# Performance work log

Measured on AMD Instinct MI355X. Metric: run time of the kernel, lower is better.

The kernel has to match this reference:

```python
import jax, jax.numpy as jnp
import numpy as np

TASKS = 32768          # init kwarg `tasks`
N_HEADS = TASKS + 1    # tasks + 1 distilled/shared head
IN_DIM, HID, OUT = 3, 100, 5


def setup_inputs() -> dict:
    key = jax.random.key(0)
    kx, k1, kb1, k2, kb2 = jax.random.split(key, 5)
    # per-task stacked parameters (equivalent to ModuleList of Linears)
    x = jax.random.normal(kx, (N_HEADS, IN_DIM), dtype=jnp.float32)
    # init scale ~ PyTorch default: U(-1/sqrt(fan_in), 1/sqrt(fan_in)); gaussian approx fine
    W1 = jax.random.normal(k1, (N_HEADS, HID, IN_DIM), dtype=jnp.float32) * (1.0 / np.sqrt(IN_DIM))
    b1 = jax.random.normal(kb1, (N_HEADS, HID), dtype=jnp.float32) * (1.0 / np.sqrt(IN_DIM))
    W2 = jax.random.normal(k2, (N_HEADS, OUT, HID), dtype=jnp.float32) * (1.0 / np.sqrt(HID))
    b2 = jax.random.normal(kb2, (N_HEADS, OUT), dtype=jnp.float32) * (1.0 / np.sqrt(HID))
    return {"x": x, "W1": W1, "b1": b1, "W2": W2, "b2": b2}


def reference(x, W1, b1, W2, b2):
    # x: (T+1, 3) -- one state vector per task head (matches x.view(tasks+1, -1))
    T1 = W1.shape[0]
    x = x.reshape(T1, -1)                                   # (T+1, 3)
    h = jax.nn.relu(jnp.einsum('thi,ti->th', W1, x) + b1)   # (T+1, 100)
    logits = jnp.einsum('toh,th->to', W2, h) + b2           # (T+1, 5)
    return jax.nn.softmax(logits, axis=-1)                  # (T+1, 5)
```

## Files before the change

### kernel.cpp

```cpp
#include <hip/hip_runtime.h>
#include <math.h>


#define N_HEADS 32769
#define IN_DIM  3
#define HID     100
#define OUT     5

__global__ __launch_bounds__(256) void distral_kernel(
    const float* __restrict__ x,
    const float* __restrict__ W1,
    const float* __restrict__ b1,
    const float* __restrict__ W2,
    const float* __restrict__ b2,
    float* __restrict__ out)
{
    const int wave = threadIdx.x >> 6;
    const int lane = threadIdx.x & 63;
    const int head = blockIdx.x * 4 + wave;
    if (head >= N_HEADS) return;

    const float x0 = x[head * 3 + 0];
    const float x1 = x[head * 3 + 1];
    const float x2 = x[head * 3 + 2];

    const float* W1h = W1 + (size_t)head * (HID * IN_DIM);
    const float* b1h = b1 + (size_t)head * HID;
    const float* W2h = W2 + (size_t)head * (OUT * HID);

    float h0, h1 = 0.0f;
    {
        const int j = lane;
        const float a0 = W1h[j * 3 + 0];
        const float a1 = W1h[j * 3 + 1];
        const float a2 = W1h[j * 3 + 2];
        h0 = fmaxf(fmaf(a0, x0, fmaf(a1, x1, fmaf(a2, x2, b1h[j]))), 0.0f);
    }
    const int j2 = lane + 64;
    const bool has2 = (j2 < HID);
    if (has2) {
        const float a0 = W1h[j2 * 3 + 0];
        const float a1 = W1h[j2 * 3 + 1];
        const float a2 = W1h[j2 * 3 + 2];
        h1 = fmaxf(fmaf(a0, x0, fmaf(a1, x1, fmaf(a2, x2, b1h[j2]))), 0.0f);
    }

    float acc[OUT];
#pragma unroll
    for (int o = 0; o < OUT; ++o) {
        float p = W2h[o * HID + lane] * h0;
        if (has2) p = fmaf(W2h[o * HID + j2], h1, p);
        acc[o] = p;
    }

#pragma unroll
    for (int off = 32; off > 0; off >>= 1) {
#pragma unroll
        for (int o = 0; o < OUT; ++o)
            acc[o] += __shfl_xor(acc[o], off, 64);
    }

    float m = -INFINITY;
#pragma unroll
    for (int o = 0; o < OUT; ++o) {
        acc[o] += b2[head * OUT + o];
        m = fmaxf(m, acc[o]);
    }
    float s = 0.0f;
#pragma unroll
    for (int o = 0; o < OUT; ++o) {
        acc[o] = __expf(acc[o] - m);
        s += acc[o];
    }
    const float inv = 1.0f / s;

    if (lane < OUT) {
        float v = (lane == 0) ? acc[0]
                : (lane == 1) ? acc[1]
                : (lane == 2) ? acc[2]
                : (lane == 3) ? acc[3]
                :               acc[4];
        out[(size_t)head * OUT + lane] = v * inv;
    }
}

extern "C" void kernel_launch(void* const* d_in, const int* in_sizes, int n_in,
                              void* d_out, int out_size, void* d_ws, size_t ws_size,
                              hipStream_t stream) {
    const float* x  = (const float*)d_in[0];
    const float* W1 = (const float*)d_in[1];
    const float* b1 = (const float*)d_in[2];
    const float* W2 = (const float*)d_in[3];
    const float* b2 = (const float*)d_in[4];
    float* out = (float*)d_out;

    const int heads_per_block = 4;
    const int blocks = (N_HEADS + heads_per_block - 1) / heads_per_block;
    distral_kernel<<<blocks, 256, 0, stream>>>(x, W1, b1, W2, b2, out);
}
```

Measured before the change: 154.5 us.

## Stage per-head weights into LDS with async global_load_lds 16-byte copies

Result: faster. 142.3 us (-7.9%).

```diff
diff --git a/kernel.cpp b/kernel.cpp
--- a/kernel.cpp
+++ b/kernel.cpp
@@ -3,9 +3,21 @@
 
 
 #define N_HEADS 32769
-#define IN_DIM  3
 #define HID     100
 #define OUT     5
+
+#define HEADS_PER_BLOCK 4
+#define FLOATS_PER_HEAD 900
+#define LDS_B1 300
+#define LDS_W2 400
+
+#define GLOBAL_AS __attribute__((address_space(1)))
+#define LDS_AS    __attribute__((address_space(3)))
+
+static __device__ __forceinline__ void async_copy16(const void* g, void* l) {
+    __builtin_amdgcn_global_load_lds((const GLOBAL_AS void*)g, (LDS_AS void*)l,
+                                     16, 0, 0);
+}
 
 __global__ __launch_bounds__(256) void distral_kernel(
     const float* __restrict__ x,
@@ -15,72 +27,92 @@
     const float* __restrict__ b2,
     float* __restrict__ out)
 {
+    __shared__ float lds[HEADS_PER_BLOCK * FLOATS_PER_HEAD];
+
     const int wave = threadIdx.x >> 6;
     const int lane = threadIdx.x & 63;
-    const int head = blockIdx.x * 4 + wave;
-    if (head >= N_HEADS) return;
+    const int head = blockIdx.x * HEADS_PER_BLOCK + wave;
+    const bool valid = (head < N_HEADS);
 
-    const float x0 = x[head * 3 + 0];
-    const float x1 = x[head * 3 + 1];
-    const float x2 = x[head * 3 + 2];
+    float* region = lds + wave * FLOATS_PER_HEAD;
 
-    const float* W1h = W1 + (size_t)head * (HID * IN_DIM);
-    const float* b1h = b1 + (size_t)head * HID;
-    const float* W2h = W2 + (size_t)head * (OUT * HID);
+    float x0 = 0.f, x1 = 0.f, x2 = 0.f;
+    float b2v[OUT] = {0.f, 0.f, 0.f, 0.f, 0.f};
 
-    float h0, h1 = 0.0f;
-    {
-        const int j = lane;
-        const float a0 = W1h[j * 3 + 0];
-        const float a1 = W1h[j * 3 + 1];
-        const float a2 = W1h[j * 3 + 2];
-        h0 = fmaxf(fmaf(a0, x0, fmaf(a1, x1, fmaf(a2, x2, b1h[j]))), 0.0f);
-    }
-    const int j2 = lane + 64;
-    const bool has2 = (j2 < HID);
-    if (has2) {
-        const float a0 = W1h[j2 * 3 + 0];
-        const float a1 = W1h[j2 * 3 + 1];
-        const float a2 = W1h[j2 * 3 + 2];
-        h1 = fmaxf(fmaf(a0, x0, fmaf(a1, x1, fmaf(a2, x2, b1h[j2]))), 0.0f);
+    if (valid) {
+        const float* W1h = W1 + (size_t)head * 300;
+        const float* b1h = b1 + (size_t)head * 100;
+        const float* W2h = W2 + (size_t)head * 500;
+
+        async_copy16(W1h + 4 * lane,            region);
+        if (lane < 11)
+            async_copy16(W1h + 256 + 4 * lane,  region + 256);
+        if (lane < 25)
+            async_copy16(b1h + 4 * lane,        region + LDS_B1);
+        async_copy16(W2h + 4 * lane,            region + LDS_W2);
+        if (lane < 61)
+            async_copy16(W2h + 256 + 4 * lane,  region + LDS_W2 + 256);
+
+        x0 = x[head * 3 + 0];
+        x1 = x[head * 3 + 1];
+        x2 = x[head * 3 + 2];
+#pragma unroll
+        for (int o = 0; o < OUT; ++o) b2v[o] = b2[head * OUT + o];
     }
 
-    float acc[OUT];
+    __syncthreads();
+
+    if (valid) {
+        const bool has2 = (lane < HID - 64);
+        float h0, h1 = 0.0f;
+        {
+            const float* r = region + 3 * lane;
+            h0 = fmaxf(fmaf(r[0], x0, fmaf(r[1], x1, fmaf(r[2], x2,
+                       region[LDS_B1 + lane]))), 0.0f);
+        }
+        if (has2) {
+            const float* r = region + 3 * (lane + 64);
+            h1 = fmaxf(fmaf(r[0], x0, fmaf(r[1], x1, fmaf(r[2], x2,
+                       region[LDS_B1 + lane + 64]))), 0.0f);
+        }
+
+        float acc[OUT];
 #pragma unroll
-    for (int o = 0; o < OUT; ++o) {
-        float p = W2h[o * HID + lane] * h0;
-        if (has2) p = fmaf(W2h[o * HID + j2], h1, p);
-        acc[o] = p;
-    }
+        for (int o = 0; o < OUT; ++o) {
+            float p = region[LDS_W2 + o * HID + lane] * h0;
+            if (has2) p = fmaf(region[LDS_W2 + o * HID + 64 + lane], h1, p);
+            acc[o] = p;
+        }
 
 #pragma unroll
-    for (int off = 32; off > 0; off >>= 1) {
+        for (int off = 32; off > 0; off >>= 1) {
 #pragma unroll
-        for (int o = 0; o < OUT; ++o)
-            acc[o] += __shfl_xor(acc[o], off, 64);
-    }
+            for (int o = 0; o < OUT; ++o)
+                acc[o] += __shfl_xor(acc[o], off, 64);
+        }
 
-    float m = -INFINITY;
+        float m = -INFINITY;
 #pragma unroll
-    for (int o = 0; o < OUT; ++o) {
-        acc[o] += b2[head * OUT + o];
-        m = fmaxf(m, acc[o]);
-    }
-    float s = 0.0f;
+        for (int o = 0; o < OUT; ++o) {
+            acc[o] += b2v[o];
+            m = fmaxf(m, acc[o]);
+        }
+        float s = 0.0f;
 #pragma unroll
-    for (int o = 0; o < OUT; ++o) {
-        acc[o] = __expf(acc[o] - m);
-        s += acc[o];
-    }
-    const float inv = 1.0f / s;
+        for (int o = 0; o < OUT; ++o) {
+            acc[o] = __expf(acc[o] - m);
+            s += acc[o];
+        }
+        const float inv = 1.0f / s;
 
-    if (lane < OUT) {
-        float v = (lane == 0) ? acc[0]
-                : (lane == 1) ? acc[1]
-                : (lane == 2) ? acc[2]
-                : (lane == 3) ? acc[3]
-                :               acc[4];
-        out[(size_t)head * OUT + lane] = v * inv;
+        if (lane < OUT) {
+            float v = (lane == 0) ? acc[0]
+                    : (lane == 1) ? acc[1]
+                    : (lane == 2) ? acc[2]
+                    : (lane == 3) ? acc[3]
+                    :               acc[4];
+            out[(size_t)head * OUT + lane] = v * inv;
+        }
     }
 }
 
@@ -94,7 +126,6 @@
     const float* b2 = (const float*)d_in[4];
     float* out = (float*)d_out;
 
-    const int heads_per_block = 4;
-    const int blocks = (N_HEADS + heads_per_block - 1) / heads_per_block;
+    const int blocks = (N_HEADS + HEADS_PER_BLOCK - 1) / HEADS_PER_BLOCK;
     distral_kernel<<<blocks, 256, 0, stream>>>(x, W1, b1, W2, b2, out);
 }
```

## Process two heads per wavefront with float4-vectorized weight loads

Applied to the files above, without the earlier changes.

New measurement: 142.1 us. 8.1% less time.

```diff
diff --git a/kernel.cpp b/kernel.cpp
--- a/kernel.cpp
+++ b/kernel.cpp
@@ -3,9 +3,9 @@
 
 
 #define N_HEADS 32769
-#define IN_DIM  3
 #define HID     100
 #define OUT     5
+#define CHUNKS  25
 
 __global__ __launch_bounds__(256) void distral_kernel(
     const float* __restrict__ x,
@@ -15,72 +15,70 @@
     const float* __restrict__ b2,
     float* __restrict__ out)
 {
-    const int wave = threadIdx.x >> 6;
     const int lane = threadIdx.x & 63;
-    const int head = blockIdx.x * 4 + wave;
-    if (head >= N_HEADS) return;
+    const int half = lane >> 5;
+    const int ll   = lane & 31;
+    const int wv   = threadIdx.x >> 6;
+
+    const int  hraw  = blockIdx.x * 8 + wv * 2 + half;
+    const bool valid = (hraw < N_HEADS);
+    const int  head  = valid ? hraw : (N_HEADS - 1);
+
+    const int c = (ll < CHUNKS) ? ll : (CHUNKS - 1);
+    const bool active = (ll < CHUNKS);
+
+    const float4* W1q = (const float4*)(W1 + (size_t)head * 300);
+    const float4* b1q = (const float4*)(b1 + (size_t)head * 100);
+    const float4* W2q = (const float4*)(W2 + (size_t)head * 500);
+
+    const float4 q0 = W1q[3 * c + 0];
+    const float4 q1 = W1q[3 * c + 1];
+    const float4 q2 = W1q[3 * c + 2];
+    const float4 bq = b1q[c];
+    float4 w2[OUT];
+#pragma unroll
+    for (int o = 0; o < OUT; ++o)
+        w2[o] = W2q[CHUNKS * o + c];
 
     const float x0 = x[head * 3 + 0];
     const float x1 = x[head * 3 + 1];
     const float x2 = x[head * 3 + 2];
+    float b2v[OUT];
+#pragma unroll
+    for (int o = 0; o < OUT; ++o) b2v[o] = b2[head * OUT + o];
 
-    const float* W1h = W1 + (size_t)head * (HID * IN_DIM);
-    const float* b1h = b1 + (size_t)head * HID;
-    const float* W2h = W2 + (size_t)head * (OUT * HID);
+    const float h0 = fmaxf(fmaf(q0.x, x0, fmaf(q0.y, x1, fmaf(q0.z, x2, bq.x))), 0.f);
+    const float h1 = fmaxf(fmaf(q0.w, x0, fmaf(q1.x, x1, fmaf(q1.y, x2, bq.y))), 0.f);
+    const float h2 = fmaxf(fmaf(q1.z, x0, fmaf(q1.w, x1, fmaf(q2.x, x2, bq.z))), 0.f);
+    const float h3 = fmaxf(fmaf(q2.y, x0, fmaf(q2.z, x1, fmaf(q2.w, x2, bq.w))), 0.f);
 
-    float h0, h1 = 0.0f;
-    {
-        const int j = lane;
-        const float a0 = W1h[j * 3 + 0];
-        const float a1 = W1h[j * 3 + 1];
-        const float a2 = W1h[j * 3 + 2];
-        h0 = fmaxf(fmaf(a0, x0, fmaf(a1, x1, fmaf(a2, x2, b1h[j]))), 0.0f);
-    }
-    const int j2 = lane + 64;
-    const bool has2 = (j2 < HID);
-    if (has2) {
-        const float a0 = W1h[j2 * 3 + 0];
-        const float a1 = W1h[j2 * 3 + 1];
-        const float a2 = W1h[j2 * 3 + 2];
-        h1 = fmaxf(fmaf(a0, x0, fmaf(a1, x1, fmaf(a2, x2, b1h[j2]))), 0.0f);
+    float logit[OUT];
+#pragma unroll
+    for (int o = 0; o < OUT; ++o) {
+        float p = fmaf(h0, w2[o].x, fmaf(h1, w2[o].y,
+                  fmaf(h2, w2[o].z, h3 * w2[o].w)));
+        p = active ? p : 0.0f;
+#pragma unroll
+        for (int m = 16; m > 0; m >>= 1)
+            p += __shfl_xor(p, m, 64);
+        logit[o] = p + b2v[o];
     }
 
-    float acc[OUT];
+    float mx = -INFINITY;
 #pragma unroll
-    for (int o = 0; o < OUT; ++o) {
-        float p = W2h[o * HID + lane] * h0;
-        if (has2) p = fmaf(W2h[o * HID + j2], h1, p);
-        acc[o] = p;
-    }
-
+    for (int o = 0; o < OUT; ++o) mx = fmaxf(mx, logit[o]);
+    float e[OUT], s = 0.0f;
 #pragma unroll
-    for (int off = 32; off > 0; off >>= 1) {
-#pragma unroll
-        for (int o = 0; o < OUT; ++o)
-            acc[o] += __shfl_xor(acc[o], off, 64);
-    }
-
-    float m = -INFINITY;
-#pragma unroll
-    for (int o = 0; o < OUT; ++o) {
-        acc[o] += b2[head * OUT + o];
-        m = fmaxf(m, acc[o]);
-    }
-    float s = 0.0f;
-#pragma unroll
-    for (int o = 0; o < OUT; ++o) {
-        acc[o] = __expf(acc[o] - m);
-        s += acc[o];
-    }
+    for (int o = 0; o < OUT; ++o) { e[o] = __expf(logit[o] - mx); s += e[o]; }
     const float inv = 1.0f / s;
 
-    if (lane < OUT) {
-        float v = (lane == 0) ? acc[0]
-                : (lane == 1) ? acc[1]
-                : (lane == 2) ? acc[2]
-                : (lane == 3) ? acc[3]
-                :               acc[4];
-        out[(size_t)head * OUT + lane] = v * inv;
+    if (valid && ll < OUT) {
+        float v = (ll == 0) ? e[0]
+                : (ll == 1) ? e[1]
+                : (ll == 2) ? e[2]
+                : (ll == 3) ? e[3]
+                :             e[4];
+        out[(size_t)head * OUT + ll] = v * inv;
     }
 }
 
@@ -94,7 +92,7 @@
     const float* b2 = (const float*)d_in[4];
     float* out = (float*)d_out;
 
-    const int heads_per_block = 4;
+    const int heads_per_block = 8;
     const int blocks = (N_HEADS + heads_per_block - 1) / heads_per_block;
     distral_kernel<<<blocks, 256, 0, stream>>>(x, W1, b1, W2, b2, out);
 }
```
